# Performance work log

Hardware: AMD Instinct MI355X
Metric: run time of the kernel (lower is better)

The kernel has to match this reference:

```python
import jax, jax.numpy as jnp
import numpy as np

TWO_PI = 2.0 * np.pi
DIST_THRESH = 0.1  # squared-distance threshold from the source


def _fourier_basis(x, y, K):
    # phase[i, l, k] = 2*pi*(k*x_i + l*y_i), k,l in 1..K, reshaped to [inchans, K*K]
    kk = jnp.arange(1, K + 1, dtype=x.dtype)  # varies along last axis (columns)
    ll = jnp.arange(1, K + 1, dtype=x.dtype)  # varies along middle axis (rows)
    phase = TWO_PI * (kk[None, None, :] * x[:, None, None]
                      + ll[None, :, None] * y[:, None, None])
    phase = phase.reshape(x.shape[0], K * K)
    return jnp.cos(phase), jnp.sin(phase)


def setup_inputs() -> dict:
    key = jax.random.key(0)
    ks = jax.random.split(key, 7)
    B, C_in, C_out, K, T = 128, 273, 270, 32, 2048
    return {
        "X": jax.random.normal(ks[0], (B, C_in, T), dtype=jnp.float32),
        "z_real": jax.random.normal(ks[1], (C_out, K * K), dtype=jnp.float32) / (32.0 * 32.0),
        "z_imag": jax.random.normal(ks[2], (C_out, K * K), dtype=jnp.float32) / (32.0 * 32.0),
        "x": jax.random.uniform(ks[3], (C_in,), dtype=jnp.float32),
        "y": jax.random.uniform(ks[4], (C_in,), dtype=jnp.float32),
        "x_drop": jax.random.uniform(ks[5], (), dtype=jnp.float32),
        "y_drop": jax.random.uniform(ks[6], (), dtype=jnp.float32),
    }


def reference(X, z_real, z_imag, x, y, x_drop, y_drop):
    K = int(np.sqrt(z_real.shape[1]))
    cos_m, sin_m = _fourier_basis(x, y, K)          # [C_in, K*K] each
    # logits over input channels: [C_out, C_in]
    a = z_real @ cos_m.T + z_imag @ sin_m.T
    # zero (not -inf) logits of channels near the drop point, as in the source
    dist2 = (x_drop - x) ** 2 + (y_drop - y) ** 2   # [C_in]
    a = jnp.where((dist2 < DIST_THRESH)[None, :], 0.0, a)
    a = jax.nn.softmax(a, axis=1)                    # [C_out, C_in]
    return jnp.einsum('oi,bit->bot', a, X)           # [B, C_out, T]
```

## Files before the change

### kernel.cpp

```cpp
#include <hip/hip_runtime.h>
#include <hip/hip_bf16.h>
#include <math.h>

typedef short s16x4 __attribute__((ext_vector_type(4)));
typedef short bf16x8 __attribute__((ext_vector_type(8)));
typedef float f32x16 __attribute__((ext_vector_type(16)));

#define C_IN 273
#define C_OUT 270
#define T_DIM 2048
#define KP 288
#define APR_STRIDE 288
#define APR_ROWS 320

#define WS_COS 0u
#define WS_SIN 1118208u
#define WS_PART 2236416u
#define WS_APERM 4743168u

#define ALD_STRIDE 592
#define A_LDS_BYTES (64 * ALD_STRIDE)
#define XBUF_BYTES 8192

__device__ __forceinline__ short f2bf(float f) {
  __hip_bfloat16 h = __float2bfloat16(f);
  short r; __builtin_memcpy(&r, &h, 2); return r;
}

__global__ void k_basis(const float* __restrict__ x, const float* __restrict__ y,
                        float* __restrict__ cosb, float* __restrict__ sinb) {
  const int i = blockIdx.x;
  const float xi = x[i], yi = y[i];
  const int base = threadIdx.x * 4;
  #pragma unroll
  for (int j = 0; j < 4; ++j) {
    const int kl = base + j;
    const float kf = (float)((kl & 31) + 1);
    const float lf = (float)((kl >> 5) + 1);
    const float ph = 6.28318530717958647692f * (kf * xi + lf * yi);
    float sn, cs;
    sincosf(ph, &sn, &cs);
    cosb[(size_t)i * 1024 + kl] = cs;
    sinb[(size_t)i * 1024 + kl] = sn;
  }
}

__global__ __launch_bounds__(256) void k_logits(const float* __restrict__ zr,
    const float* __restrict__ zi, const float* __restrict__ cosb,
    const float* __restrict__ sinb, float* __restrict__ part) {
  const int tx = threadIdx.x & 15, ty = threadIdx.x >> 4;
  const int ibase = blockIdx.x * 64 + tx * 4;
  const int obase = blockIdx.y * 64 + ty * 4;
  const int kl0 = (int)blockIdx.z * 128;
  int oc[4], ic[4];
  #pragma unroll
  for (int a = 0; a < 4; ++a) {
    oc[a] = min(obase + a, C_OUT - 1);
    ic[a] = min(ibase + a, C_IN - 1);
  }
  float acc[4][4] = {};
  for (int kl = kl0; kl < kl0 + 128; kl += 4) {
    float4 zr4[4], zi4[4], cb4[4], sb4[4];
    #pragma unroll
    for (int a = 0; a < 4; ++a) {
      zr4[a] = *(const float4*)(zr + (size_t)oc[a] * 1024 + kl);
      zi4[a] = *(const float4*)(zi + (size_t)oc[a] * 1024 + kl);
    }
    #pragma unroll
    for (int b = 0; b < 4; ++b) {
      cb4[b] = *(const float4*)(cosb + (size_t)ic[b] * 1024 + kl);
      sb4[b] = *(const float4*)(sinb + (size_t)ic[b] * 1024 + kl);
    }
    #pragma unroll
    for (int a = 0; a < 4; ++a)
      #pragma unroll
      for (int b = 0; b < 4; ++b)
        acc[a][b] += zr4[a].x * cb4[b].x + zr4[a].y * cb4[b].y
                   + zr4[a].z * cb4[b].z + zr4[a].w * cb4[b].w
                   + zi4[a].x * sb4[b].x + zi4[a].y * sb4[b].y
                   + zi4[a].z * sb4[b].z + zi4[a].w * sb4[b].w;
  }
  #pragma unroll
  for (int a = 0; a < 4; ++a)
    #pragma unroll
    for (int b = 0; b < 4; ++b) {
      const int o = obase + a, i = ibase + b;
      if (o < C_OUT && i < C_IN)
        part[((size_t)blockIdx.z * 272 + o) * 288 + i] = acc[a][b];
    }
}

__global__ __launch_bounds__(256) void k_softmax(const float* __restrict__ part,
    const float* __restrict__ x, const float* __restrict__ y,
    const float* __restrict__ xdp, const float* __restrict__ ydp,
    __hip_bfloat16* __restrict__ aperm) {
  const int o = blockIdx.x;
  const int tid = threadIdx.x;
  if (o >= C_OUT) {
    for (int s = tid; s < KP; s += 256)
      aperm[(size_t)o * APR_STRIDE + s] = __float2bfloat16(0.f);
    return;
  }
  __shared__ float red[8];
  const float xd = xdp[0], yd = ydp[0];
  const int i0 = tid, i1 = tid + 256;
  float v0, v1 = 0.f;
  {
    float s = 0.f;
    #pragma unroll
    for (int c = 0; c < 8; ++c) s += part[((size_t)c * 272 + o) * 288 + i0];
    const float dx = xd - x[i0], dy = yd - y[i0];
    v0 = (dx * dx + dy * dy < 0.1f) ? 0.f : s;
  }
  const bool has1 = (i1 < C_IN);
  if (has1) {
    float s = 0.f;
    #pragma unroll
    for (int c = 0; c < 8; ++c) s += part[((size_t)c * 272 + o) * 288 + i1];
    const float dx = xd - x[i1], dy = yd - y[i1];
    v1 = (dx * dx + dy * dy < 0.1f) ? 0.f : s;
  }
  float mv = has1 ? fmaxf(v0, v1) : v0;
  #pragma unroll
  for (int off = 32; off >= 1; off >>= 1) mv = fmaxf(mv, __shfl_down(mv, off));
  if ((tid & 63) == 0) red[tid >> 6] = mv;
  __syncthreads();
  const float M = fmaxf(fmaxf(red[0], red[1]), fmaxf(red[2], red[3]));
  const float e0 = expf(v0 - M);
  const float e1 = has1 ? expf(v1 - M) : 0.f;
  float sv = e0 + e1;
  #pragma unroll
  for (int off = 32; off >= 1; off >>= 1) sv += __shfl_down(sv, off);
  __syncthreads();
  if ((tid & 63) == 0) red[4 + (tid >> 6)] = sv;
  __syncthreads();
  const float S = red[4] + red[5] + red[6] + red[7];
  const float inv = 1.0f / S;
  {
    const int s = (i0 & ~3) | ((i0 & 3) ^ ((i0 >> 2) & 3));
    aperm[(size_t)o * APR_STRIDE + s] = __float2bfloat16(e0 * inv);
  }
  if (i1 < KP) {
    const int s = (i1 & ~3) | ((i1 & 3) ^ ((i1 >> 2) & 3));
    aperm[(size_t)o * APR_STRIDE + s] = __float2bfloat16(has1 ? e1 * inv : 0.f);
  }
}

__device__ __forceinline__ void load_chunk(const float* __restrict__ Xb, int ch,
                                           int t_base, int tid, float4 (&r)[4]) {
  const int k4 = tid & 7, t4 = tid >> 3;
  const int t = t_base + t4 * 4;
  #pragma unroll
  for (int rr = 0; rr < 4; ++rr) {
    const int i = ch * 32 + k4 * 4 + rr;
    float4 v = make_float4(0.f, 0.f, 0.f, 0.f);
    if (i < C_IN) v = *(const float4*)(Xb + (size_t)i * T_DIM + t);
    r[rr] = v;
  }
}

__device__ __forceinline__ void write_chunk(char* __restrict__ xb, int tid,
                                            const float4 (&r)[4]) {
  const int k4 = tid & 7, t4 = tid >> 3;
  const int tb = t4 >> 2, c4 = t4 & 3;
  #pragma unroll
  for (int rr = 0; rr < 4; ++rr) {
    const int j = rr ^ (k4 & 3);
    s16x4 p;
    p[0] = f2bf(r[rr].x); p[1] = f2bf(r[rr].y);
    p[2] = f2bf(r[rr].z); p[3] = f2bf(r[rr].w);
    *(s16x4*)(xb + (k4 * 8 + tb) * 128 + j * 32 + c4 * 8) = p;
  }
}

__global__ __launch_bounds__(256) void k_gemm(const float* __restrict__ X,
    const __hip_bfloat16* __restrict__ aperm, float* __restrict__ out) {
  __shared__ __align__(16) char smem[A_LDS_BYTES + 2 * XBUF_BYTES];
  const int tid = threadIdx.x;
  const int lane = tid & 63, w = tid >> 6;

  const int bid = blockIdx.x;
  const int xcd = bid & 7, slot = bid >> 3;
  const int bat = slot / 80;
  const int idx = slot - bat * 80;
  const int b   = bat * 8 + xcd;
  const int oy  = idx % 5;
  const int tx  = idx / 5;
  const int o_base = oy * 64;
  const int t_base = tx * 128;
  const float* Xb = X + (size_t)b * C_IN * T_DIM;

  {
    const int row = tid >> 2, q = tid & 3;
    const float4* src = (const float4*)((const char*)(aperm + (size_t)(o_base + row) * APR_STRIDE) + q * 144);
    float4* dst = (float4*)(smem + row * ALD_STRIDE + q * 144);
    #pragma unroll
    for (int v = 0; v < 9; ++v) dst[v] = src[v];
  }

  f32x16 acc[2] = {};
  const unsigned smem_u = (unsigned)(unsigned long long)(uintptr_t)smem;
  const unsigned xlds0 = smem_u + A_LDS_BYTES;
  const int lg = lane >> 4, l16 = lane & 15, l32 = lane & 31, lh = lane >> 5;
  const unsigned bconst = (unsigned)((lg >> 1) * 2048 + (lg & 1) * 128 + w * 256 + l16 * 8);

  char* xb0 = smem + A_LDS_BYTES;
  char* xb1 = smem + A_LDS_BYTES + XBUF_BYTES;

  float4 rA[4], rB[4];
  load_chunk(Xb, 0, t_base, tid, rA);
  load_chunk(Xb, 1, t_base, tid, rB);
  write_chunk(xb0, tid, rA);
  __syncthreads();

  #define COMPUTE(CH, BUFSEL)                                                      \
    {                                                                              \
      const unsigned xb = xlds0 + (BUFSEL) * XBUF_BYTES + bconst;                  \
      const char* arow0 = smem + l32 * ALD_STRIDE + ((CH) * 32) * 2 + lh * 16;     \
      _Pragma("unroll")                                                            \
      for (int kk = 0; kk < 32; kk += 16) {                                        \
        bf16x8 A0 = *(const bf16x8*)(arow0 + kk * 2);                              \
        bf16x8 A1 = *(const bf16x8*)(arow0 + 32 * ALD_STRIDE + kk * 2);            \
        s16x4 t0, t1;                                                              \
        const unsigned a0 = xb + kk * 256;                                         \
        asm volatile("ds_read_b64_tr_b16 %0, %1" : "=v"(t0) : "v"(a0));            \
        asm volatile("ds_read_b64_tr_b16 %0, %1 offset:1024" : "=v"(t1) : "v"(a0));\
        asm volatile("s_waitcnt lgkmcnt(0)" ::: "memory");                         \
        __builtin_amdgcn_sched_barrier(0);                                         \
        bf16x8 B0;                                                                 \
        B0[0] = t0[0]; B0[1] = t0[1]; B0[2] = t0[2]; B0[3] = t0[3];                \
        B0[4] = t1[0]; B0[5] = t1[1]; B0[6] = t1[2]; B0[7] = t1[3];                \
        acc[0] = __builtin_amdgcn_mfma_f32_32x32x16_bf16(A0, B0, acc[0], 0, 0, 0); \
        acc[1] = __builtin_amdgcn_mfma_f32_32x32x16_bf16(A1, B0, acc[1], 0, 0, 0); \
      }                                                                            \
    }

  for (int ch = 0; ch < 9; ch += 2) {
    if (ch + 2 < 9) load_chunk(Xb, ch + 2, t_base, tid, rA);
    COMPUTE(ch, 0)
    if (ch + 1 < 9) write_chunk(xb1, tid, rB);
    __syncthreads();
    if (ch + 1 < 9) {
      if (ch + 3 < 9) load_chunk(Xb, ch + 3, t_base, tid, rB);
      COMPUTE(ch + 1, 1)
      if (ch + 2 < 9) write_chunk(xb0, tid, rA);
      __syncthreads();
    }
  }
  #undef COMPUTE

  float* outb = out + (size_t)b * C_OUT * T_DIM;
  #pragma unroll
  for (int m = 0; m < 2; ++m)
    #pragma unroll
    for (int r = 0; r < 16; ++r) {
      const int o = o_base + m * 32 + (r & 3) + 8 * (r >> 2) + 4 * lh;
      if (o < C_OUT) {
        const int t = t_base + w * 32 + l32;
        outb[(size_t)o * T_DIM + t] = acc[m][r];
      }
    }
}

extern "C" void kernel_launch(void* const* d_in, const int* in_sizes, int n_in,
                              void* d_out, int out_size, void* d_ws, size_t ws_size,
                              hipStream_t stream) {
  const float* X  = (const float*)d_in[0];
  const float* zr = (const float*)d_in[1];
  const float* zi = (const float*)d_in[2];
  const float* x  = (const float*)d_in[3];
  const float* y  = (const float*)d_in[4];
  const float* xd = (const float*)d_in[5];
  const float* yd = (const float*)d_in[6];
  float* out = (float*)d_out;
  char* ws = (char*)d_ws;
  float* cosb = (float*)(ws + WS_COS);
  float* sinb = (float*)(ws + WS_SIN);
  float* part = (float*)(ws + WS_PART);
  __hip_bfloat16* aperm = (__hip_bfloat16*)(ws + WS_APERM);

  k_basis<<<dim3(273), dim3(256), 0, stream>>>(x, y, cosb, sinb);
  k_logits<<<dim3(5, 5, 8), dim3(256), 0, stream>>>(zr, zi, cosb, sinb, part);
  k_softmax<<<dim3(APR_ROWS), dim3(256), 0, stream>>>(part, x, y, xd, yd, aperm);
  k_gemm<<<dim3(10240), dim3(256), 0, stream>>>(X, aperm, out);
}
```

Baseline: 348.0 us.

## Pre-transpose X to bf16 T-major workspace and use direct-load MFMA GEMM

Adds a pass that transposes and converts X into a bf16 buffer with time as the row index and channels contiguous. A new GEMM then loads MFMA fragments straight from global memory with a register triple buffer, bypassing LDS staging. The softmax gains a flag to skip the swizzle permutation in this path. The new path only runs when the workspace holds about 156 MB, and it adds an extra full read and write of X plus strided gathers in the transpose.

New measurement: 481.4 us. 1.38x slower.

```diff
diff --git a/kernel.cpp b/kernel.cpp
--- a/kernel.cpp
+++ b/kernel.cpp
@@ -17,6 +17,15 @@
 #define WS_SIN 1118208u
 #define WS_PART 2236416u
 #define WS_APERM 4743168u
+
+#define XT_ROW 576u
+#define XT_PER_B 1179648u
+#define XT_TOTAL 150994944u
+#define WS2_COS   150994944u
+#define WS2_SIN   152113152u
+#define WS2_PART  153231360u
+#define WS2_APERM 155738112u
+#define WS2_END   155922432u
 
 #define ALD_STRIDE 592
 #define A_LDS_BYTES (64 * ALD_STRIDE)
@@ -93,7 +102,7 @@
 __global__ __launch_bounds__(256) void k_softmax(const float* __restrict__ part,
     const float* __restrict__ x, const float* __restrict__ y,
     const float* __restrict__ xdp, const float* __restrict__ ydp,
-    __hip_bfloat16* __restrict__ aperm) {
+    __hip_bfloat16* __restrict__ aperm, int perm) {
   const int o = blockIdx.x;
   const int tid = threadIdx.x;
   if (o >= C_OUT) {
@@ -137,13 +146,86 @@
   const float S = red[4] + red[5] + red[6] + red[7];
   const float inv = 1.0f / S;
   {
-    const int s = (i0 & ~3) | ((i0 & 3) ^ ((i0 >> 2) & 3));
+    const int s = perm ? ((i0 & ~3) | ((i0 & 3) ^ ((i0 >> 2) & 3))) : i0;
     aperm[(size_t)o * APR_STRIDE + s] = __float2bfloat16(e0 * inv);
   }
   if (i1 < KP) {
-    const int s = (i1 & ~3) | ((i1 & 3) ^ ((i1 >> 2) & 3));
+    const int s = perm ? ((i1 & ~3) | ((i1 & 3) ^ ((i1 >> 2) & 3))) : i1;
     aperm[(size_t)o * APR_STRIDE + s] = __float2bfloat16(has1 ? e1 * inv : 0.f);
   }
+}
+
+__global__ __launch_bounds__(256) void k_trans(const float* __restrict__ X,
+                                               char* __restrict__ Xt) {
+  const int t = blockIdx.x * 256 + threadIdx.x;
+  const int b = blockIdx.y;
+  const float* Xb = X + (size_t)b * C_IN * T_DIM;
+  char* row = Xt + (size_t)b * XT_PER_B + (size_t)t * XT_ROW;
+  #pragma unroll 4
+  for (int i0 = 0; i0 < KP; i0 += 8) {
+    bf16x8 p;
+    #pragma unroll
+    for (int ii = 0; ii < 8; ++ii) {
+      const int i = i0 + ii;
+      const float v = (i < C_IN) ? Xb[(size_t)i * T_DIM + t] : 0.f;
+      p[ii] = f2bf(v);
+    }
+    *(bf16x8*)(row + i0 * 2) = p;
+  }
+}
+
+__global__ __launch_bounds__(256) void k_gemm2(const __hip_bfloat16* __restrict__ aperm,
+    const char* __restrict__ Xt, float* __restrict__ out) {
+  const int tid = threadIdx.x;
+  const int lane = tid & 63, w = tid >> 6;
+  const int l32 = lane & 31, lh = lane >> 5;
+  const int tb = blockIdx.x;
+  const int ob = blockIdx.y;
+  const int b  = blockIdx.z;
+
+  const int t = tb * 128 + w * 32 + l32;
+  const char* Brow  = Xt + (size_t)b * XT_PER_B + (size_t)t * XT_ROW + lh * 16;
+  const char* Arow0 = (const char*)aperm + (size_t)(ob * 96 + l32) * 576 + lh * 16;
+  const char* Arow1 = Arow0 + 32 * 576;
+  const char* Arow2 = Arow0 + 64 * 576;
+
+  f32x16 acc[3] = {};
+  bf16x8 Bf[3], Af[3][3];
+
+  Bf[0] = *(const bf16x8*)(Brow);
+  Af[0][0] = *(const bf16x8*)(Arow0);
+  Af[0][1] = *(const bf16x8*)(Arow1);
+  Af[0][2] = *(const bf16x8*)(Arow2);
+  Bf[1] = *(const bf16x8*)(Brow + 32);
+  Af[1][0] = *(const bf16x8*)(Arow0 + 32);
+  Af[1][1] = *(const bf16x8*)(Arow1 + 32);
+  Af[1][2] = *(const bf16x8*)(Arow2 + 32);
+
+  #pragma unroll
+  for (int kk = 0; kk < 18; ++kk) {
+    const int cur = kk % 3;
+    if (kk + 2 < 18) {
+      const int nxt = (kk + 2) % 3;
+      const int off = (kk + 2) * 32;
+      Bf[nxt]    = *(const bf16x8*)(Brow  + off);
+      Af[nxt][0] = *(const bf16x8*)(Arow0 + off);
+      Af[nxt][1] = *(const bf16x8*)(Arow1 + off);
+      Af[nxt][2] = *(const bf16x8*)(Arow2 + off);
+    }
+    acc[0] = __builtin_amdgcn_mfma_f32_32x32x16_bf16(Af[cur][0], Bf[cur], acc[0], 0, 0, 0);
+    acc[1] = __builtin_amdgcn_mfma_f32_32x32x16_bf16(Af[cur][1], Bf[cur], acc[1], 0, 0, 0);
+    acc[2] = __builtin_amdgcn_mfma_f32_32x32x16_bf16(Af[cur][2], Bf[cur], acc[2], 0, 0, 0);
+  }
+
+  float* outb = out + (size_t)b * C_OUT * T_DIM;
+  #pragma unroll
+  for (int mi = 0; mi < 3; ++mi)
+    #pragma unroll
+    for (int r = 0; r < 16; ++r) {
+      const int o = ob * 96 + mi * 32 + (r & 3) + 8 * (r >> 2) + 4 * lh;
+      if (o < C_OUT)
+        outb[(size_t)o * T_DIM + t] = acc[mi][r];
+    }
 }
 
 __device__ __forceinline__ void load_chunk(const float* __restrict__ Xb, int ch,
@@ -173,12 +255,11 @@
   }
 }
 
-__global__ __launch_bounds__(256) void k_gemm(const float* __restrict__ X,
+__global__ __launch_bounds__(256) void k_gemm_old(const float* __restrict__ X,
     const __hip_bfloat16* __restrict__ aperm, float* __restrict__ out) {
   __shared__ __align__(16) char smem[A_LDS_BYTES + 2 * XBUF_BYTES];
   const int tid = threadIdx.x;
   const int lane = tid & 63, w = tid >> 6;
-
   const int bid = blockIdx.x;
   const int xcd = bid & 7, slot = bid >> 3;
   const int bat = slot / 80;
@@ -274,13 +355,29 @@
   const float* yd = (const float*)d_in[6];
   float* out = (float*)d_out;
   char* ws = (char*)d_ws;
-  float* cosb = (float*)(ws + WS_COS);
-  float* sinb = (float*)(ws + WS_SIN);
-  float* part = (float*)(ws + WS_PART);
-  __hip_bfloat16* aperm = (__hip_bfloat16*)(ws + WS_APERM);
-
-  k_basis<<<dim3(273), dim3(256), 0, stream>>>(x, y, cosb, sinb);
-  k_logits<<<dim3(5, 5, 8), dim3(256), 0, stream>>>(zr, zi, cosb, sinb, part);
-  k_softmax<<<dim3(APR_ROWS), dim3(256), 0, stream>>>(part, x, y, xd, yd, aperm);
-  k_gemm<<<dim3(10240), dim3(256), 0, stream>>>(X, aperm, out);
-}
+
+  const bool big = ws_size >= (size_t)WS2_END;
+  if (big) {
+    float* cosb = (float*)(ws + WS2_COS);
+    float* sinb = (float*)(ws + WS2_SIN);
+    float* part = (float*)(ws + WS2_PART);
+    __hip_bfloat16* aperm = (__hip_bfloat16*)(ws + WS2_APERM);
+    char* Xt = ws;
+
+    k_basis<<<dim3(273), dim3(256), 0, stream>>>(x, y, cosb, sinb);
+    k_logits<<<dim3(5, 5, 8), dim3(256), 0, stream>>>(zr, zi, cosb, sinb, part);
+    k_softmax<<<dim3(APR_ROWS), dim3(256), 0, stream>>>(part, x, y, xd, yd, aperm, 0);
+    k_trans<<<dim3(8, 128), dim3(256), 0, stream>>>(X, Xt);
+    k_gemm2<<<dim3(16, 3, 128), dim3(256), 0, stream>>>(aperm, Xt, out);
+  } else {
+    float* cosb = (float*)(ws + WS_COS);
+    float* sinb = (float*)(ws + WS_SIN);
+    float* part = (float*)(ws + WS_PART);
+    __hip_bfloat16* aperm = (__hip_bfloat16*)(ws + WS_APERM);
+
+    k_basis<<<dim3(273), dim3(256), 0, stream>>>(x, y, cosb, sinb);
+    k_logits<<<dim3(5, 5, 8), dim3(256), 0, stream>>>(zr, zi, cosb, sinb, part);
+    k_softmax<<<dim3(APR_ROWS), dim3(256), 0, stream>>>(part, x, y, xd, yd, aperm, 1);
+    k_gemm_old<<<dim3(10240), dim3(256), 0, stream>>>(X, aperm, out);
+  }
+}
```
